# Kernel optimization log

Hardware: AMD Instinct MI355X
Metric: run time of the kernel (lower is better)

Reference implementation:

```python
import jax, jax.numpy as jnp
import numpy as np

HEAD_SIZE = 64
N_EMBED = 1024
THETA = 10000.0


def _rope_cos_sin(T, dim):
    # freqs = 1/theta^(2i/dim), i in [0, dim//2)
    freqs = 1.0 / (THETA ** (jnp.arange(0, dim, 2, dtype=jnp.float32) / dim))  # (dim//2,)
    angles = jnp.arange(T, dtype=jnp.float32)[:, None] * freqs[None, :]        # (T, dim//2)
    return jnp.cos(angles), jnp.sin(angles)


def _apply_rope(q, cos, sin):
    # q: (B, T, hs); interpret consecutive pairs as complex (even=real, odd=imag)
    B, T, hs = q.shape
    qr = q.reshape(B, T, hs // 2, 2)
    ev, od = qr[..., 0], qr[..., 1]
    out_ev = ev * cos - od * sin
    out_od = ev * sin + od * cos
    return jnp.stack([out_ev, out_od], axis=-1).reshape(B, T, hs)


def setup_inputs() -> dict:
    key = jax.random.key(0)
    ks = jax.random.split(key, 7)
    B, T = 4, 2048
    s = 1.0 / np.sqrt(N_EMBED)
    return {
        "x": jax.random.normal(ks[0], (B, T, N_EMBED), dtype=jnp.float32),
        "mask": jnp.ones((B, T), dtype=jnp.int32),
        "Wq": jax.random.uniform(ks[1], (N_EMBED, HEAD_SIZE), jnp.float32, -s, s),
        "bq": jax.random.uniform(ks[2], (HEAD_SIZE,), jnp.float32, -s, s),
        "Wk": jax.random.uniform(ks[3], (N_EMBED, HEAD_SIZE), jnp.float32, -s, s),
        "bk": jax.random.uniform(ks[4], (HEAD_SIZE,), jnp.float32, -s, s),
        "Wv": jax.random.uniform(ks[5], (N_EMBED, HEAD_SIZE), jnp.float32, -s, s),
        "bv": jax.random.uniform(ks[6], (HEAD_SIZE,), jnp.float32, -s, s),
    }


def reference(x, mask, Wq, bq, Wk, bk, Wv, bv):
    B, T, C = x.shape
    Q = x @ Wq + bq  # (B, T, hs)
    K = x @ Wk + bk
    V = x @ Wv + bv

    cos, sin = _rope_cos_sin(T, HEAD_SIZE)
    Q = _apply_rope(Q, cos, sin)
    K = _apply_rope(K, cos, sin)

    causal = jnp.triu(jnp.ones((T, T), dtype=bool), k=1)[None, :, :]  # (1, T, T)
    pad = (mask == 0)[:, :, None]                                     # (B, T, 1) masks rows
    attn_mask = causal | pad                                          # (B, T, T)

    scores = jnp.einsum('btd,bsd->bts', Q, K) * (C ** -0.5)
    scores = jnp.where(attn_mask, -jnp.inf, scores)
    attn = jax.nn.softmax(scores, axis=-1)
    # dropout in eval mode: identity
    return jnp.einsum('bts,bsd->btd', attn, V)
```

## Files before the change

kernel.cpp:

```cpp
#include <hip/hip_runtime.h>
#include <math.h>


typedef __attribute__((ext_vector_type(8))) short short8v;
typedef __attribute__((ext_vector_type(4))) short short4v;
typedef __attribute__((ext_vector_type(4))) float f32x4;

__device__ __forceinline__ unsigned short f2bf(float f){
  unsigned int u = __float_as_uint(f);
  u += 0x7fffu + ((u >> 16) & 1u);
  return (unsigned short)(u >> 16);
}
__device__ __forceinline__ float bf2f(unsigned short h){
  return __uint_as_float(((unsigned int)h) << 16);
}
__device__ __forceinline__ f32x4 mfma16(short8v a, short8v b, f32x4 c){
  return __builtin_amdgcn_mfma_f32_16x16x32_bf16(a, b, c, 0, 0, 0);
}


__global__ __launch_bounds__(256) void prep_k(
    const float* __restrict__ Wq, const float* __restrict__ Wk, const float* __restrict__ Wv,
    unsigned short* __restrict__ WThi, unsigned short* __restrict__ WTlo,
    float2* __restrict__ rope)
{
  const int tid = blockIdx.x * 256 + threadIdx.x;
  #pragma unroll
  for (int it = 0; it < 3; ++it){
    const int idx = tid + 65536 * it;
    const int k = idx / 192;
    const int n = idx - k * 192;
    const float v = (n < 64) ? Wq[k*64 + n] : (n < 128 ? Wk[k*64 + n - 64] : Wv[k*64 + n - 128]);
    const unsigned short hi = f2bf(v);
    WThi[n*1024 + k] = hi;
    WTlo[n*1024 + k] = f2bf(v - bf2f(hi));
  }
  const int p = tid & 31, tt = tid >> 5;
  const float freq = exp2f((float)p * -0.4152410118609203f);
  float s, c;
  sincosf((float)tt * freq, &s, &c);
  rope[tid] = make_float2(c, s);
}

__global__ __launch_bounds__(512) void qkv_k(
    const float* __restrict__ x,
    const unsigned short* __restrict__ WThi, const unsigned short* __restrict__ WTlo,
    const float* __restrict__ bq, const float* __restrict__ bk, const float* __restrict__ bv,
    const float2* __restrict__ rope,
    unsigned short* __restrict__ Qb, unsigned short* __restrict__ Kb,
    unsigned short* __restrict__ VT)
{
  __shared__ __align__(16) unsigned short XAh[32][72], XAl[32][72];
  __shared__ __align__(16) unsigned short WTh[192][72], WTl[192][72];

  const int t = threadIdx.x;
  const int w = t >> 6, l = t & 63;
  const int h = w & 1, nh = w >> 1;
  const int g = l >> 4, c16 = l & 15;
  const int m0 = blockIdx.x * 32;

  f32x4 acc[3];
  #pragma unroll
  for (int nt = 0; nt < 3; ++nt) acc[nt] = (f32x4){0.f, 0.f, 0.f, 0.f};

  const int xr = t >> 4, xc = (t & 15) * 4;

  for (int k0 = 0; k0 < 1024; k0 += 64){
    __syncthreads();
    {
      const float4 a4 = *(const float4*)&x[(m0 + xr) * 1024 + k0 + xc];
      const float f[4] = {a4.x, a4.y, a4.z, a4.w};
      union { short4v v; unsigned short u[4]; } hh, ll;
      #pragma unroll
      for (int j = 0; j < 4; ++j){
        hh.u[j] = f2bf(f[j]);
        ll.u[j] = f2bf(f[j] - bf2f(hh.u[j]));
      }
      *(short4v*)&XAh[xr][xc] = hh.v;
      *(short4v*)&XAl[xr][xc] = ll.v;
    }
    #pragma unroll
    for (int a = 0; a < 3; ++a){
      const int ch = t + 512 * a;
      const int wn = ch >> 3, wk = (ch & 7) * 8;
      *(short8v*)&WTh[wn][wk] = *(const short8v*)&WThi[wn*1024 + k0 + wk];
      *(short8v*)&WTl[wn][wk] = *(const short8v*)&WTlo[wn*1024 + k0 + wk];
    }
    __syncthreads();
    #pragma unroll
    for (int ks = 0; ks < 2; ++ks){
      const short8v ah  = *(const short8v*)&XAh[16*h + c16][ks*32 + g*8];
      const short8v al2 = *(const short8v*)&XAl[16*h + c16][ks*32 + g*8];
      #pragma unroll
      for (int nt = 0; nt < 3; ++nt){
        const int wr = 48*nh + 16*nt + c16;
        const short8v bh = *(const short8v*)&WTh[wr][ks*32 + g*8];
        const short8v bl = *(const short8v*)&WTl[wr][ks*32 + g*8];
        acc[nt] = mfma16(ah, bh, acc[nt]);
        acc[nt] = mfma16(ah, bl, acc[nt]);
        acc[nt] = mfma16(al2, bh, acc[nt]);
      }
    }
  }

  #pragma unroll
  for (int nt = 0; nt < 3; ++nt){
    const int c = 48*nh + 16*nt + c16;
    const int m = c >> 6, cm = c & 63;
    const float* bptr = (m == 0) ? bq : (m == 1 ? bk : bv);
    const float bias = bptr[cm];
    #pragma unroll
    for (int i = 0; i < 4; ++i){
      const int gr = m0 + 16*h + 4*g + i;
      float v = acc[nt][i] + bias;
      const float other = __shfl_xor(v, 1);
      if (m < 2){
        const float2 cs = rope[(gr & 2047) * 32 + (cm >> 1)];
        v = (c & 1) ? fmaf(v, cs.x,  other * cs.y)
                    : fmaf(v, cs.x, -other * cs.y);
      }
      if (m == 0)      Qb[gr*64 + cm] = f2bf(v);
      else if (m == 1) Kb[gr*64 + cm] = f2bf(v);
      else             VT[((size_t)(gr >> 11) * 64 + cm) * 2048 + (gr & 2047)] = f2bf(v);
    }
  }
}

__global__ __launch_bounds__(512) void attn_k(
    const unsigned short* __restrict__ Qb, const unsigned short* __restrict__ Kb,
    const unsigned short* __restrict__ VT, float* __restrict__ out)
{
  __shared__ __align__(16) unsigned short Kh[64][72];
  __shared__ __align__(16) unsigned short Vh[64][72];
  __shared__ __align__(16) unsigned short Ph[8][16][24];
  __shared__ float Om[2][3][16][68];
  __shared__ float Ml[2][3][16][2];

  const int t = threadIdx.x;
  const int w = t >> 6, l = t & 63;
  const int h = w & 1, kh = w >> 1;
  const int g = l >> 4, c16 = l & 15;
  const int b = blockIdx.y;
  const int q0 = (63 - (int)blockIdx.x) * 32;
  const size_t bT = (size_t)b * 2048;

  short8v qh[2];
  {
    const size_t qoff = (bT + q0 + 16*h + c16) * 64 + g*8;
    qh[0] = *(const short8v*)&Qb[qoff];
    qh[1] = *(const short8v*)&Qb[qoff + 32];
  }

  f32x4 acc[4];
  #pragma unroll
  for (int nt = 0; nt < 4; ++nt) acc[nt] = (f32x4){0.f, 0.f, 0.f, 0.f};
  float m_run[4], l_run[4];
  #pragma unroll
  for (int i = 0; i < 4; ++i){ m_run[i] = -INFINITY; l_run[i] = 0.f; }

  const int sr = t >> 3, sc = (t & 7) * 8;
  const int nk = q0 / 64 + 1;

  short8v kreg = *(const short8v*)&Kb[(bT + sr) * 64 + sc];
  short8v vreg = *(const short8v*)&VT[((size_t)b * 64 + sr) * 2048 + sc];

  for (int kt = 0; kt < nk; ++kt){
    __syncthreads();
    *(short8v*)&Kh[sr][sc] = kreg;
    *(short8v*)&Vh[sr][sc] = vreg;
    if (kt + 1 < nk){
      const int k1 = (kt + 1) * 64;
      kreg = *(const short8v*)&Kb[(bT + k1 + sr) * 64 + sc];
      vreg = *(const short8v*)&VT[((size_t)b * 64 + sr) * 2048 + k1 + sc];
    }
    __syncthreads();

    const int k0 = kt * 64;
    f32x4 z = (f32x4){0.f, 0.f, 0.f, 0.f};
    {
      const short8v kb0 = *(const short8v*)&Kh[16*kh + c16][g*8];
      const short8v kb1 = *(const short8v*)&Kh[16*kh + c16][32 + g*8];
      z = mfma16(qh[0], kb0, z);
      z = mfma16(qh[1], kb1, z);
    }

    float sv[4];
    #pragma unroll
    for (int i = 0; i < 4; ++i){
      float v = z[i] * 0.03125f;
      if (kt == nk - 1){
        const int keyg = k0 + 16*kh + c16;
        const int qg = q0 + 16*h + 4*g + i;
        if (keyg > qg) v = -INFINITY;
      }
      sv[i] = v;
    }

    float al[4];
    #pragma unroll
    for (int i = 0; i < 4; ++i){
      float pm = sv[i];
      pm = fmaxf(pm, __shfl_xor(pm, 1));
      pm = fmaxf(pm, __shfl_xor(pm, 2));
      pm = fmaxf(pm, __shfl_xor(pm, 4));
      pm = fmaxf(pm, __shfl_xor(pm, 8));
      const float mnew = fmaxf(m_run[i], pm);
      const float msafe = fmaxf(mnew, -1e30f);
      al[i] = expf(m_run[i] - msafe);
      const float p0 = expf(sv[i] - msafe);
      float ps = p0;
      ps += __shfl_xor(ps, 1);
      ps += __shfl_xor(ps, 2);
      ps += __shfl_xor(ps, 4);
      ps += __shfl_xor(ps, 8);
      l_run[i] = l_run[i] * al[i] + ps;
      m_run[i] = mnew;
      Ph[w][4*g + i][c16] = f2bf(p0);
    }

    #pragma unroll
    for (int nt = 0; nt < 4; ++nt)
      #pragma unroll
      for (int i = 0; i < 4; ++i) acc[nt][i] *= al[i];

    short8v pa;
    if (g < 2) pa = *(const short8v*)&Ph[w][c16][g*8];
    else       pa = (short8v){0,0,0,0,0,0,0,0};
    const int kcol = 16*kh + 8*(g & 1);
    #pragma unroll
    for (int nt = 0; nt < 4; ++nt){
      const short8v vb = *(const short8v*)&Vh[16*nt + c16][kcol];
      acc[nt] = mfma16(pa, vb, acc[nt]);
    }
  }

  if (kh > 0){
    #pragma unroll
    for (int nt = 0; nt < 4; ++nt)
      #pragma unroll
      for (int i = 0; i < 4; ++i)
        Om[h][kh-1][4*g + i][16*nt + c16] = acc[nt][i];
    if (c16 == 0){
      #pragma unroll
      for (int i = 0; i < 4; ++i){
        Ml[h][kh-1][4*g + i][0] = m_run[i];
        Ml[h][kh-1][4*g + i][1] = l_run[i];
      }
    }
  }
  __syncthreads();
  if (kh == 0){
    float es[4], e[3][4], linv[4];
    #pragma unroll
    for (int i = 0; i < 4; ++i){
      float mo[3], lo[3];
      float mm = m_run[i];
      #pragma unroll
      for (int j = 0; j < 3; ++j){
        mo[j] = Ml[h][j][4*g + i][0];
        lo[j] = Ml[h][j][4*g + i][1];
        mm = fmaxf(mm, mo[j]);
      }
      es[i] = expf(m_run[i] - mm);
      float lt = l_run[i] * es[i];
      #pragma unroll
      for (int j = 0; j < 3; ++j){
        e[j][i] = (mo[j] == -INFINITY) ? 0.f : expf(mo[j] - mm);
        lt += lo[j] * e[j][i];
      }
      linv[i] = 1.f / lt;
    }
    #pragma unroll
    for (int nt = 0; nt < 4; ++nt)
      #pragma unroll
      for (int i = 0; i < 4; ++i){
        float v = acc[nt][i] * es[i];
        #pragma unroll
        for (int j = 0; j < 3; ++j)
          v += Om[h][j][4*g + i][16*nt + c16] * e[j][i];
        out[(bT + q0 + 16*h + 4*g + i) * 64 + 16*nt + c16] = v * linv[i];
      }
  }
}

extern "C" void kernel_launch(void* const* d_in, const int* in_sizes, int n_in,
                              void* d_out, int out_size, void* d_ws, size_t ws_size,
                              hipStream_t stream) {
  (void)in_sizes; (void)n_in; (void)out_size; (void)ws_size;
  const float* x    = (const float*)d_in[0];
  const float* Wq   = (const float*)d_in[2];
  const float* bq   = (const float*)d_in[3];
  const float* Wk   = (const float*)d_in[4];
  const float* bk   = (const float*)d_in[5];
  const float* Wv   = (const float*)d_in[6];
  const float* bv   = (const float*)d_in[7];
  float* out = (float*)d_out;

  const size_t NROW = 8192;
  unsigned short* Qb   = (unsigned short*)d_ws;
  unsigned short* Kb   = Qb  + NROW * 64;
  unsigned short* VT   = Kb  + NROW * 64;
  unsigned short* WThi = VT  + NROW * 64;
  unsigned short* WTlo = WThi + 192 * 1024;
  float2*         rope = (float2*)(WTlo + 192 * 1024);

  prep_k<<<dim3(256), dim3(256), 0, stream>>>(Wq, Wk, Wv, WThi, WTlo, rope);
  qkv_k<<<dim3(256), dim3(512), 0, stream>>>(x, WThi, WTlo, bq, bk, bv, rope,
                                             Qb, Kb, VT);
  attn_k<<<dim3(64, 4), dim3(512), 0, stream>>>(Qb, Kb, VT, out);
}
```

Baseline: 162.7 us.

## Retile weight prep, QKV projection and attention to use direct register loads

The weight transpose now goes through a shared-memory tile, so global reads and writes are coalesced. The QKV GEMM is retiled to 64 rows by 96 columns over a 2D grid. The attention kernel doubles its block size to 16 waves, each handling a 16-key slice of a 128-key tile, and drops the shared K/V staging and its barriers in favour of direct per-lane global loads with K prefetched one tile ahead. This removes the per-iteration syncthreads and halves the loop trip count. The cost is that more redundant global traffic now relies on cache hits, and the final merge across 8 partial states grows in size.

```diff
diff --git a/kernel.cpp b/kernel.cpp
--- a/kernel.cpp
+++ b/kernel.cpp
@@ -3,7 +3,6 @@
 
 
 typedef __attribute__((ext_vector_type(8))) short short8v;
-typedef __attribute__((ext_vector_type(4))) short short4v;
 typedef __attribute__((ext_vector_type(4))) float f32x4;
 
 __device__ __forceinline__ unsigned short f2bf(float f){
@@ -24,22 +23,46 @@
     unsigned short* __restrict__ WThi, unsigned short* __restrict__ WTlo,
     float2* __restrict__ rope)
 {
-  const int tid = blockIdx.x * 256 + threadIdx.x;
-  #pragma unroll
-  for (int it = 0; it < 3; ++it){
-    const int idx = tid + 65536 * it;
-    const int k = idx / 192;
-    const int n = idx - k * 192;
-    const float v = (n < 64) ? Wq[k*64 + n] : (n < 128 ? Wk[k*64 + n - 64] : Wv[k*64 + n - 128]);
-    const unsigned short hi = f2bf(v);
-    WThi[n*1024 + k] = hi;
-    WTlo[n*1024 + k] = f2bf(v - bf2f(hi));
-  }
-  const int p = tid & 31, tt = tid >> 5;
-  const float freq = exp2f((float)p * -0.4152410118609203f);
-  float s, c;
-  sincosf((float)tt * freq, &s, &c);
-  rope[tid] = make_float2(c, s);
+  __shared__ __align__(16) unsigned short Th[64][72], Tl[64][72];
+  const int t  = threadIdx.x;
+  const int k0 = blockIdx.x * 64;
+  const int mtx = blockIdx.y;
+  const float* Wsrc = (mtx == 0) ? Wq : (mtx == 1 ? Wk : Wv);
+  const int n0 = mtx * 64;
+
+  {
+    const int r  = t >> 2;
+    const int cb = (t & 3) * 16;
+    #pragma unroll
+    for (int j4 = 0; j4 < 4; ++j4){
+      const float4 v4 = *(const float4*)&Wsrc[(k0 + r) * 64 + cb + j4 * 4];
+      const float f[4] = {v4.x, v4.y, v4.z, v4.w};
+      #pragma unroll
+      for (int u = 0; u < 4; ++u){
+        const unsigned short hi = f2bf(f[u]);
+        Th[cb + j4*4 + u][r] = hi;
+        Tl[cb + j4*4 + u][r] = f2bf(f[u] - bf2f(hi));
+      }
+    }
+  }
+  __syncthreads();
+  {
+    const int n  = t >> 2;
+    const int kc = (t & 3) * 16;
+    #pragma unroll
+    for (int c = 0; c < 2; ++c){
+      *(short8v*)&WThi[(size_t)(n0 + n) * 1024 + k0 + kc + c*8] = *(const short8v*)&Th[n][kc + c*8];
+      *(short8v*)&WTlo[(size_t)(n0 + n) * 1024 + k0 + kc + c*8] = *(const short8v*)&Tl[n][kc + c*8];
+    }
+  }
+  const int gtid = (blockIdx.y * 16 + blockIdx.x) * 256 + t;
+  for (int idx = gtid; idx < 65536; idx += 48 * 256){
+    const int p = idx & 31, tt = idx >> 5;
+    const float freq = exp2f((float)p * -0.4152410118609203f);
+    float s, c;
+    sincosf((float)tt * freq, &s, &c);
+    rope[idx] = make_float2(c, s);
+  }
 }
 
 __global__ __launch_bounds__(512) void qkv_k(
@@ -50,50 +73,55 @@
     unsigned short* __restrict__ Qb, unsigned short* __restrict__ Kb,
     unsigned short* __restrict__ VT)
 {
-  __shared__ __align__(16) unsigned short XAh[32][72], XAl[32][72];
-  __shared__ __align__(16) unsigned short WTh[192][72], WTl[192][72];
+  __shared__ __align__(16) unsigned short XAh[64][72], XAl[64][72];
+  __shared__ __align__(16) unsigned short WTh[96][72], WTl[96][72];
 
   const int t = threadIdx.x;
   const int w = t >> 6, l = t & 63;
-  const int h = w & 1, nh = w >> 1;
+  const int rg = w & 3, cg = w >> 2;
   const int g = l >> 4, c16 = l & 15;
-  const int m0 = blockIdx.x * 32;
+  const int m0 = blockIdx.x * 64;
+  const int n0 = blockIdx.y * 96;
 
   f32x4 acc[3];
   #pragma unroll
   for (int nt = 0; nt < 3; ++nt) acc[nt] = (f32x4){0.f, 0.f, 0.f, 0.f};
 
-  const int xr = t >> 4, xc = (t & 15) * 4;
+  const int xr = t >> 3, xc = (t & 7) * 8;
 
   for (int k0 = 0; k0 < 1024; k0 += 64){
     __syncthreads();
     {
-      const float4 a4 = *(const float4*)&x[(m0 + xr) * 1024 + k0 + xc];
-      const float f[4] = {a4.x, a4.y, a4.z, a4.w};
-      union { short4v v; unsigned short u[4]; } hh, ll;
-      #pragma unroll
-      for (int j = 0; j < 4; ++j){
+      const float* xp = &x[(size_t)(m0 + xr) * 1024 + k0 + xc];
+      const float4 a4 = *(const float4*)xp;
+      const float4 b4 = *(const float4*)(xp + 4);
+      const float f[8] = {a4.x, a4.y, a4.z, a4.w, b4.x, b4.y, b4.z, b4.w};
+      union { short8v v; unsigned short u[8]; } hh, ll;
+      #pragma unroll
+      for (int j = 0; j < 8; ++j){
         hh.u[j] = f2bf(f[j]);
         ll.u[j] = f2bf(f[j] - bf2f(hh.u[j]));
       }
-      *(short4v*)&XAh[xr][xc] = hh.v;
-      *(short4v*)&XAl[xr][xc] = ll.v;
+      *(short8v*)&XAh[xr][xc] = hh.v;
+      *(short8v*)&XAl[xr][xc] = ll.v;
     }
     #pragma unroll
     for (int a = 0; a < 3; ++a){
       const int ch = t + 512 * a;
-      const int wn = ch >> 3, wk = (ch & 7) * 8;
-      *(short8v*)&WTh[wn][wk] = *(const short8v*)&WThi[wn*1024 + k0 + wk];
-      *(short8v*)&WTl[wn][wk] = *(const short8v*)&WTlo[wn*1024 + k0 + wk];
+      const int cc = (ch < 768) ? ch : ch - 768;
+      const int wn = cc >> 3, wk = (cc & 7) * 8;
+      const size_t go = (size_t)(n0 + wn) * 1024 + k0 + wk;
+      if (ch < 768) *(short8v*)&WTh[wn][wk] = *(const short8v*)&WThi[go];
+      else          *(short8v*)&WTl[wn][wk] = *(const short8v*)&WTlo[go];
     }
     __syncthreads();
     #pragma unroll
     for (int ks = 0; ks < 2; ++ks){
-      const short8v ah  = *(const short8v*)&XAh[16*h + c16][ks*32 + g*8];
-      const short8v al2 = *(const short8v*)&XAl[16*h + c16][ks*32 + g*8];
+      const short8v ah  = *(const short8v*)&XAh[16*rg + c16][ks*32 + g*8];
+      const short8v al2 = *(const short8v*)&XAl[16*rg + c16][ks*32 + g*8];
       #pragma unroll
       for (int nt = 0; nt < 3; ++nt){
-        const int wr = 48*nh + 16*nt + c16;
+        const int wr = 48*cg + 16*nt + c16;
         const short8v bh = *(const short8v*)&WTh[wr][ks*32 + g*8];
         const short8v bl = *(const short8v*)&WTl[wr][ks*32 + g*8];
         acc[nt] = mfma16(ah, bh, acc[nt]);
@@ -105,13 +133,13 @@
 
   #pragma unroll
   for (int nt = 0; nt < 3; ++nt){
-    const int c = 48*nh + 16*nt + c16;
+    const int c = n0 + 48*cg + 16*nt + c16;
     const int m = c >> 6, cm = c & 63;
     const float* bptr = (m == 0) ? bq : (m == 1 ? bk : bv);
     const float bias = bptr[cm];
     #pragma unroll
     for (int i = 0; i < 4; ++i){
-      const int gr = m0 + 16*h + 4*g + i;
+      const int gr = m0 + 16*rg + 4*g + i;
       float v = acc[nt][i] + bias;
       const float other = __shfl_xor(v, 1);
       if (m < 2){
@@ -119,22 +147,20 @@
         v = (c & 1) ? fmaf(v, cs.x,  other * cs.y)
                     : fmaf(v, cs.x, -other * cs.y);
       }
-      if (m == 0)      Qb[gr*64 + cm] = f2bf(v);
-      else if (m == 1) Kb[gr*64 + cm] = f2bf(v);
+      if (m == 0)      Qb[(size_t)gr*64 + cm] = f2bf(v);
+      else if (m == 1) Kb[(size_t)gr*64 + cm] = f2bf(v);
       else             VT[((size_t)(gr >> 11) * 64 + cm) * 2048 + (gr & 2047)] = f2bf(v);
     }
   }
 }
 
-__global__ __launch_bounds__(512) void attn_k(
+__global__ __launch_bounds__(1024) void attn_k(
     const unsigned short* __restrict__ Qb, const unsigned short* __restrict__ Kb,
     const unsigned short* __restrict__ VT, float* __restrict__ out)
 {
-  __shared__ __align__(16) unsigned short Kh[64][72];
-  __shared__ __align__(16) unsigned short Vh[64][72];
-  __shared__ __align__(16) unsigned short Ph[8][16][24];
-  __shared__ float Om[2][3][16][68];
-  __shared__ float Ml[2][3][16][2];
+  __shared__ __align__(16) unsigned short Ph[16][16][24];
+  __shared__ float Om[2][7][16][68];
+  __shared__ float Ml[2][7][16][2];
 
   const int t = threadIdx.x;
   const int w = t >> 6, l = t & 63;
@@ -144,12 +170,15 @@
   const int q0 = (63 - (int)blockIdx.x) * 32;
   const size_t bT = (size_t)b * 2048;
 
-  short8v qh[2];
+  short8v qh0, qh1;
   {
     const size_t qoff = (bT + q0 + 16*h + c16) * 64 + g*8;
-    qh[0] = *(const short8v*)&Qb[qoff];
-    qh[1] = *(const short8v*)&Qb[qoff + 32];
-  }
+    qh0 = *(const short8v*)&Qb[qoff];
+    qh1 = *(const short8v*)&Qb[qoff + 32];
+  }
+
+  const unsigned short* Kbase = &Kb[(bT + 16*kh + c16) * 64 + g*8];
+  const unsigned short* Vbase = &VT[((size_t)b*64 + c16) * 2048 + 16*kh + 8*(g & 1)];
 
   f32x4 acc[4];
   #pragma unroll
@@ -158,31 +187,28 @@
   #pragma unroll
   for (int i = 0; i < 4; ++i){ m_run[i] = -INFINITY; l_run[i] = 0.f; }
 
-  const int sr = t >> 3, sc = (t & 7) * 8;
-  const int nk = q0 / 64 + 1;
-
-  short8v kreg = *(const short8v*)&Kb[(bT + sr) * 64 + sc];
-  short8v vreg = *(const short8v*)&VT[((size_t)b * 64 + sr) * 2048 + sc];
+  const int nk = q0 / 128 + 1;
+  const short8v zero8 = (short8v){0,0,0,0,0,0,0,0};
+
+  short8v kb0c = *(const short8v*)&Kbase[0];
+  short8v kb1c = *(const short8v*)&Kbase[32];
 
   for (int kt = 0; kt < nk; ++kt){
-    __syncthreads();
-    *(short8v*)&Kh[sr][sc] = kreg;
-    *(short8v*)&Vh[sr][sc] = vreg;
-    if (kt + 1 < nk){
-      const int k1 = (kt + 1) * 64;
-      kreg = *(const short8v*)&Kb[(bT + k1 + sr) * 64 + sc];
-      vreg = *(const short8v*)&VT[((size_t)b * 64 + sr) * 2048 + k1 + sc];
-    }
-    __syncthreads();
-
-    const int k0 = kt * 64;
+    const int k0 = kt * 128;
+    short8v vb0 = zero8, vb1 = zero8, vb2 = zero8, vb3 = zero8;
+    if (g < 2){
+      vb0 = *(const short8v*)&Vbase[k0];
+      vb1 = *(const short8v*)&Vbase[k0 + 32768];
+      vb2 = *(const short8v*)&Vbase[k0 + 65536];
+      vb3 = *(const short8v*)&Vbase[k0 + 98304];
+    }
+    const int kn = (kt + 1 < nk ? kt + 1 : kt) * 128;
+    const short8v kb0n = *(const short8v*)&Kbase[(size_t)kn * 64];
+    const short8v kb1n = *(const short8v*)&Kbase[(size_t)kn * 64 + 32];
+
     f32x4 z = (f32x4){0.f, 0.f, 0.f, 0.f};
-    {
-      const short8v kb0 = *(const short8v*)&Kh[16*kh + c16][g*8];
-      const short8v kb1 = *(const short8v*)&Kh[16*kh + c16][32 + g*8];
-      z = mfma16(qh[0], kb0, z);
-      z = mfma16(qh[1], kb1, z);
-    }
+    z = mfma16(qh0, kb0c, z);
+    z = mfma16(qh1, kb1c, z);
 
     float sv[4];
     #pragma unroll
@@ -223,15 +249,14 @@
       #pragma unroll
       for (int i = 0; i < 4; ++i) acc[nt][i] *= al[i];
 
-    short8v pa;
+    short8v pa = zero8;
     if (g < 2) pa = *(const short8v*)&Ph[w][c16][g*8];
-    else       pa = (short8v){0,0,0,0,0,0,0,0};
-    const int kcol = 16*kh + 8*(g & 1);
-    #pragma unroll
-    for (int nt = 0; nt < 4; ++nt){
-      const short8v vb = *(const short8v*)&Vh[16*nt + c16][kcol];
-      acc[nt] = mfma16(pa, vb, acc[nt]);
-    }
+    acc[0] = mfma16(pa, vb0, acc[0]);
+    acc[1] = mfma16(pa, vb1, acc[1]);
+    acc[2] = mfma16(pa, vb2, acc[2]);
+    acc[3] = mfma16(pa, vb3, acc[3]);
+
+    kb0c = kb0n; kb1c = kb1n;
   }
 
   if (kh > 0){
@@ -250,13 +275,13 @@
   }
   __syncthreads();
   if (kh == 0){
-    float es[4], e[3][4], linv[4];
+    float es[4], e[7][4], linv[4];
     #pragma unroll
     for (int i = 0; i < 4; ++i){
-      float mo[3], lo[3];
+      float mo[7], lo[7];
       float mm = m_run[i];
       #pragma unroll
-      for (int j = 0; j < 3; ++j){
+      for (int j = 0; j < 7; ++j){
         mo[j] = Ml[h][j][4*g + i][0];
         lo[j] = Ml[h][j][4*g + i][1];
         mm = fmaxf(mm, mo[j]);
@@ -264,7 +289,7 @@
       es[i] = expf(m_run[i] - mm);
       float lt = l_run[i] * es[i];
       #pragma unroll
-      for (int j = 0; j < 3; ++j){
+      for (int j = 0; j < 7; ++j){
         e[j][i] = (mo[j] == -INFINITY) ? 0.f : expf(mo[j] - mm);
         lt += lo[j] * e[j][i];
       }
@@ -276,7 +301,7 @@
       for (int i = 0; i < 4; ++i){
         float v = acc[nt][i] * es[i];
         #pragma unroll
-        for (int j = 0; j < 3; ++j)
+        for (int j = 0; j < 7; ++j)
           v += Om[h][j][4*g + i][16*nt + c16] * e[j][i];
         out[(bT + q0 + 16*h + 4*g + i) * 64 + 16*nt + c16] = v * linv[i];
       }
@@ -304,8 +329,8 @@
   unsigned short* WTlo = WThi + 192 * 1024;
   float2*         rope = (float2*)(WTlo + 192 * 1024);
 
-  prep_k<<<dim3(256), dim3(256), 0, stream>>>(Wq, Wk, Wv, WThi, WTlo, rope);
-  qkv_k<<<dim3(256), dim3(512), 0, stream>>>(x, WThi, WTlo, bq, bk, bv, rope,
-                                             Qb, Kb, VT);
-  attn_k<<<dim3(64, 4), dim3(512), 0, stream>>>(Qb, Kb, VT, out);
-}
+  prep_k<<<dim3(16, 3), dim3(256), 0, stream>>>(Wq, Wk, Wv, WThi, WTlo, rope);
+  qkv_k<<<dim3(128, 2), dim3(512), 0, stream>>>(x, WThi, WTlo, bq, bk, bv, rope,
+                                                Qb, Kb, VT);
+  attn_k<<<dim3(64, 4), dim3(1024), 0, stream>>>(Qb, Kb, VT, out);
+}
```

New measurement: 164.6 us. No clear change (+1.2%).
